# Performance work log

Measured on AMD Instinct MI355X. Metric: run time of the kernel, lower is better.

## Reference

```python
import jax, jax.numpy as jnp
import numpy as np

# N: batch rows of x, D: inner dim, E: output columns of sparse A, PER_COL: nnz per column
N, D, E, PER_COL = 64, 4096, 8192, 128
NNZ = E * PER_COL  # 1,048,576 nonzeros, stored sorted by column (CSC-like)


def setup_inputs() -> dict:
    key = jax.random.key(0)
    k1, k2, k3 = jax.random.split(key, 3)
    x = jax.random.normal(k1, (N, D), dtype=jnp.float32)
    values = jax.random.normal(k2, (NNZ,), dtype=jnp.float32)  # A.values (log-space entries)
    rows = jax.random.randint(k3, (NNZ,), 0, D, dtype=jnp.int32)  # A.indices[0]: row id in D
    # A.indices[1] / col_indptrs: column-sorted segment ids; every column non-empty
    col_ids = jnp.repeat(jnp.arange(E, dtype=jnp.int32), PER_COL)
    return {"x": x, "values": values, "rows": rows, "col_ids": col_ids}


def reference(x, values, rows, col_ids):
    # expansion[k, n] = A.values[k] + x[n, rows[k]]   (nnz leading so segment ops apply)
    expansion = values[:, None] + x.T[rows]                       # [NNZ, N]
    # segment max over each column's nnz block (== segment_csr(..., 'max'))
    m = jax.ops.segment_max(expansion, col_ids, num_segments=E)   # [E, N]
    # stable sum-exp offset by per-segment max, then log (== segment_csr(..., 'sum'))
    s = jax.ops.segment_sum(jnp.exp(expansion - m[col_ids]), col_ids, num_segments=E)  # [E, N]
    return (m + jnp.log(s)).T                                     # [N, E]
```

## Files before the change

### kernel.cpp

```cpp
#include <hip/hip_runtime.h>

#define NB  64
#define D_  4096
#define E_  8192
#define PC_ 128

#define LOG2E 1.4426950408889634f
#define LN2   0.6931471805599453f


typedef float vfloat2 __attribute__((ext_vector_type(2)));
#if __has_builtin(__builtin_amdgcn_cvt_pk_f32_fp8) && \
    __has_builtin(__builtin_amdgcn_cvt_pk_fp8_f32)
#define HW_FP8 1
#else
#define HW_FP8 0
#endif

__device__ __forceinline__ unsigned enc_e4m3(float y) {
    unsigned b = __float_as_uint(y);
    int t = (int)((b + 0x00080000u) >> 20) - 960;
    t = (t < 8) ? 0 : t;
    t = (t > 127) ? 127 : t;
    return (unsigned)t;
}
__device__ __forceinline__ float dec_e4m3(unsigned u) {
    return (u >= 8u) ? __uint_as_float((u + 960u) << 20) : 0.0f;
}

__global__ __launch_bounds__(256) void k_prep(const float* __restrict__ x,
                                              const float* __restrict__ values,
                                              const int*   __restrict__ rows,
                                              unsigned* __restrict__ y4,
                                              int2*     __restrict__ meta) {
    const int b = blockIdx.x;
    if (b < D_ / 64) {
        __shared__ float ld[64][65];
        const int wv = threadIdx.x >> 6, lane = threadIdx.x & 63;
        const int d0 = b * 64;
#pragma unroll
        for (int jj = 0; jj < 16; ++jj) {
            int n = wv + 4 * jj;
            ld[lane][n] = x[n * D_ + d0 + lane];
        }
        __syncthreads();
#pragma unroll
        for (int it = 0; it < 4; ++it) {
            int item = it * 256 + threadIdx.x;
            int dd = item >> 4, j = item & 15;
            float e0  = __builtin_amdgcn_exp2f(ld[dd][j]      * LOG2E);
            float e16 = __builtin_amdgcn_exp2f(ld[dd][j + 16] * LOG2E);
            float e32 = __builtin_amdgcn_exp2f(ld[dd][j + 32] * LOG2E);
            float e48 = __builtin_amdgcn_exp2f(ld[dd][j + 48] * LOG2E);
            unsigned p;
#if HW_FP8
            p = __builtin_amdgcn_cvt_pk_fp8_f32(e0,  e16, 0, false);
            p = __builtin_amdgcn_cvt_pk_fp8_f32(e32, e48, p, true);
#else
            p = enc_e4m3(e0) | (enc_e4m3(e16) << 8) |
                (enc_e4m3(e32) << 16) | (enc_e4m3(e48) << 24);
#endif
            y4[(d0 + dd) * 16 + j] = p;
        }
    } else {
        int i = (b - D_ / 64) * 1024 + threadIdx.x * 4;
        int4   r4 = *(const int4*)(rows + i);
        float4 v4 = *(const float4*)(values + i);
        int4 s0, s1;
        s0.x = r4.x; s0.y = __float_as_int(__builtin_amdgcn_exp2f(v4.x * LOG2E));
        s0.z = r4.y; s0.w = __float_as_int(__builtin_amdgcn_exp2f(v4.y * LOG2E));
        s1.x = r4.z; s1.y = __float_as_int(__builtin_amdgcn_exp2f(v4.z * LOG2E));
        s1.z = r4.w; s1.w = __float_as_int(__builtin_amdgcn_exp2f(v4.w * LOG2E));
        ((int4*)(meta + i))[0] = s0;
        ((int4*)(meta + i))[1] = s1;
    }
}

__global__ __launch_bounds__(256, 4) void k_acc(const unsigned* __restrict__ y4,
                                                const int2*  __restrict__ meta,
                                                float* __restrict__ out) {
    const int wv   = threadIdx.x >> 6;
    const int lane = threadIdx.x & 63;
    const int q    = lane >> 4;
    const int j    = lane & 15;
    const int e    = blockIdx.x * 4 + wv;
    const int2* __restrict__ mp = meta + e * PC_ + 32 * q;

    int4 mm[16];
#pragma unroll
    for (int u = 0; u < 16; ++u)
        mm[u] = *(const int4*)(mp + 2 * u);

    float ax = 0.f, ay = 0.f, az = 0.f, aw = 0.f;
#pragma unroll
    for (int u = 0; u < 16; ++u) {
        unsigned g0 = y4[((unsigned)mm[u].x << 4) + j];
        unsigned g1 = y4[((unsigned)mm[u].z << 4) + j];
        float w0 = __int_as_float(mm[u].y);
        float w1 = __int_as_float(mm[u].w);
#if HW_FP8
        vfloat2 a01 = __builtin_amdgcn_cvt_pk_f32_fp8(g0, false);
        vfloat2 a23 = __builtin_amdgcn_cvt_pk_f32_fp8(g0, true);
        vfloat2 b01 = __builtin_amdgcn_cvt_pk_f32_fp8(g1, false);
        vfloat2 b23 = __builtin_amdgcn_cvt_pk_f32_fp8(g1, true);
        float a0 = a01[0], a1 = a01[1], a2 = a23[0], a3 = a23[1];
        float b0 = b01[0], b1 = b01[1], b2 = b23[0], b3 = b23[1];
#else
        float a0 = dec_e4m3(g0 & 0xff), a1 = dec_e4m3((g0 >> 8) & 0xff);
        float a2 = dec_e4m3((g0 >> 16) & 0xff), a3 = dec_e4m3(g0 >> 24);
        float b0 = dec_e4m3(g1 & 0xff), b1 = dec_e4m3((g1 >> 8) & 0xff);
        float b2 = dec_e4m3((g1 >> 16) & 0xff), b3 = dec_e4m3(g1 >> 24);
#endif
        ax = __builtin_fmaf(w0, a0, ax);
        ay = __builtin_fmaf(w0, a1, ay);
        az = __builtin_fmaf(w0, a2, az);
        aw = __builtin_fmaf(w0, a3, aw);
        ax = __builtin_fmaf(w1, b0, ax);
        ay = __builtin_fmaf(w1, b1, ay);
        az = __builtin_fmaf(w1, b2, az);
        aw = __builtin_fmaf(w1, b3, aw);
    }

    ax += __shfl_xor(ax, 16); ax += __shfl_xor(ax, 32);
    ay += __shfl_xor(ay, 16); ay += __shfl_xor(ay, 32);
    az += __shfl_xor(az, 16); az += __shfl_xor(az, 32);
    aw += __shfl_xor(aw, 16); aw += __shfl_xor(aw, 32);

    if (q == 0) {
        out[j        * E_ + e] = LN2 * __builtin_amdgcn_logf(ax);
        out[(j + 16) * E_ + e] = LN2 * __builtin_amdgcn_logf(ay);
        out[(j + 32) * E_ + e] = LN2 * __builtin_amdgcn_logf(az);
        out[(j + 48) * E_ + e] = LN2 * __builtin_amdgcn_logf(aw);
    }
}

extern "C" void kernel_launch(void* const* d_in, const int* in_sizes, int n_in,
                              void* d_out, int out_size, void* d_ws, size_t ws_size,
                              hipStream_t stream) {
    const float* x      = (const float*)d_in[0];
    const float* values = (const float*)d_in[1];
    const int*   rows   = (const int*)d_in[2];
    float* out = (float*)d_out;

    char* ws = (char*)d_ws;
    unsigned* y4   = (unsigned*)ws;
    int2*     meta = (int2*)(ws + (512 << 10));

    k_prep<<<D_ / 64 + (E_ * PC_) / 1024, 256, 0, stream>>>(x, values, rows, y4, meta);
    k_acc <<<E_ / 4, 256, 0, stream>>>(y4, meta, out);
}
```

Baseline: 22.24 us.

## Bucket column nonzeros by row chunk and gather from LDS-staged tiles

The prep kernel now sorts each column's nonzeros into four row-range buckets using shared-memory atomic counters, with a fixed capacity per bucket and padding to multiples of eight. The accumulate kernel runs 1024-thread blocks covering 32 columns each. It stages one 64KB chunk of the packed fp8 exp(x) table into LDS at a time, and each wave walks its bucket of nonzeros against that chunk. The aim is to turn random global/L2 gathers into LDS gathers. The costs are a doubled metadata footprint, only one block per CU, extra barriers, and entries silently clamped if any bucket exceeds its capacity of 64.

```diff
diff --git a/kernel.cpp b/kernel.cpp
--- a/kernel.cpp
+++ b/kernel.cpp
@@ -8,6 +8,11 @@
 #define LOG2E 1.4426950408889634f
 #define LN2   0.6931471805599453f
 
+
+#define CH_LOG  10
+#define CH_ROWS 1024
+#define NCH     4
+#define CAP     64
 
 typedef float vfloat2 __attribute__((ext_vector_type(2)));
 #if __has_builtin(__builtin_amdgcn_cvt_pk_f32_fp8) && \
@@ -32,7 +37,8 @@
                                               const float* __restrict__ values,
                                               const int*   __restrict__ rows,
                                               unsigned* __restrict__ y4,
-                                              int2*     __restrict__ meta) {
+                                              unsigned* __restrict__ counts,
+                                              int2*     __restrict__ msort) {
     const int b = blockIdx.x;
     if (b < D_ / 64) {
         __shared__ float ld[64][65];
@@ -63,74 +69,137 @@
             y4[(d0 + dd) * 16 + j] = p;
         }
     } else {
-        int i = (b - D_ / 64) * 1024 + threadIdx.x * 4;
-        int4   r4 = *(const int4*)(rows + i);
-        float4 v4 = *(const float4*)(values + i);
-        int4 s0, s1;
-        s0.x = r4.x; s0.y = __float_as_int(__builtin_amdgcn_exp2f(v4.x * LOG2E));
-        s0.z = r4.y; s0.w = __float_as_int(__builtin_amdgcn_exp2f(v4.y * LOG2E));
-        s1.x = r4.z; s1.y = __float_as_int(__builtin_amdgcn_exp2f(v4.z * LOG2E));
-        s1.z = r4.w; s1.w = __float_as_int(__builtin_amdgcn_exp2f(v4.w * LOG2E));
-        ((int4*)(meta + i))[0] = s0;
-        ((int4*)(meta + i))[1] = s1;
+        __shared__ int cnts[4][NCH];
+        const int wv = threadIdx.x >> 6, lane = threadIdx.x & 63;
+        const int e = (b - D_ / 64) * 4 + wv;
+        if (lane < NCH) cnts[wv][lane] = 0;
+        __syncthreads();
+
+        const int base = e * PC_;
+        int   rA = rows[base + lane],      rB = rows[base + 64 + lane];
+        float wA = __builtin_amdgcn_exp2f(values[base + lane]      * LOG2E);
+        float wB = __builtin_amdgcn_exp2f(values[base + 64 + lane] * LOG2E);
+        int cA = rA >> CH_LOG, cB = rB >> CH_LOG;
+        int sA = atomicAdd(&cnts[wv][cA], 1);
+        int sB = atomicAdd(&cnts[wv][cB], 1);
+        sA = min(sA, CAP - 1); sB = min(sB, CAP - 1);
+        int2* mcol = msort + e * (NCH * CAP);
+        mcol[cA * CAP + sA] = make_int2(rA, __float_as_int(wA));
+        mcol[cB * CAP + sB] = make_int2(rB, __float_as_int(wB));
+        __syncthreads();
+
+        if (lane < 32) {
+            int c = lane >> 3, p = lane & 7;
+            int cnt = cnts[wv][c];
+            int padded = (cnt + 7) & ~7;
+            if (cnt + p < padded)
+                mcol[c * CAP + cnt + p] = make_int2(c << CH_LOG, 0);
+        }
+        if (lane == 0) {
+            unsigned t0 = (unsigned)(cnts[wv][0] + 7) >> 3;
+            unsigned t1 = (unsigned)(cnts[wv][1] + 7) >> 3;
+            unsigned t2 = (unsigned)(cnts[wv][2] + 7) >> 3;
+            unsigned t3 = (unsigned)(cnts[wv][3] + 7) >> 3;
+            counts[e] = t0 | (t1 << 8) | (t2 << 16) | (t3 << 24);
+        }
     }
 }
 
-__global__ __launch_bounds__(256, 4) void k_acc(const unsigned* __restrict__ y4,
-                                                const int2*  __restrict__ meta,
-                                                float* __restrict__ out) {
-    const int wv   = threadIdx.x >> 6;
-    const int lane = threadIdx.x & 63;
+__global__ __launch_bounds__(1024, 1) void k_acc(const unsigned* __restrict__ y4,
+                                                 const unsigned* __restrict__ counts,
+                                                 const int2*  __restrict__ msort,
+                                                 float* __restrict__ out) {
+    __shared__ unsigned ylds[CH_ROWS * 16];
+    const int tid  = threadIdx.x;
+    const int wv   = tid >> 6;
+    const int lane = tid & 63;
     const int q    = lane >> 4;
     const int j    = lane & 15;
-    const int e    = blockIdx.x * 4 + wv;
-    const int2* __restrict__ mp = meta + e * PC_ + 32 * q;
-
-    int4 mm[16];
+    const int e0   = blockIdx.x * 32 + wv;
+    const int e1   = e0 + 16;
+
+    const unsigned cp0 = counts[e0], cp1 = counts[e1];
+    const int2* __restrict__ m0 = msort + e0 * (NCH * CAP);
+    const int2* __restrict__ m1 = msort + e1 * (NCH * CAP);
+
+    float a0x = 0.f, a0y = 0.f, a0z = 0.f, a0w = 0.f;
+    float a1x = 0.f, a1y = 0.f, a1z = 0.f, a1w = 0.f;
+
+    for (int c = 0; c < NCH; ++c) {
+        __syncthreads();
+        {
+            const uint4* __restrict__ src =
+                (const uint4*)(y4 + c * (CH_ROWS * 16));
+            uint4* dst = (uint4*)ylds;
 #pragma unroll
-    for (int u = 0; u < 16; ++u)
-        mm[u] = *(const int4*)(mp + 2 * u);
-
-    float ax = 0.f, ay = 0.f, az = 0.f, aw = 0.f;
-#pragma unroll
-    for (int u = 0; u < 16; ++u) {
-        unsigned g0 = y4[((unsigned)mm[u].x << 4) + j];
-        unsigned g1 = y4[((unsigned)mm[u].z << 4) + j];
-        float w0 = __int_as_float(mm[u].y);
-        float w1 = __int_as_float(mm[u].w);
+            for (int r = 0; r < 4; ++r)
+                dst[tid + r * 1024] = src[tid + r * 1024];
+        }
+        __syncthreads();
+
+#define WALK(MP, CP, AX, AY, AZ, AW)                                          \
+        {                                                                     \
+            const int T = (int)((CP >> (8 * c)) & 0xffu);                     \
+            const int2* __restrict__ mc = MP + c * CAP;                       \
+            for (int t = 0; t < T; ++t) {                                     \
+                int4 m4 = *(const int4*)(mc + 8 * t + 2 * q);                 \
+                unsigned gA = ylds[(((unsigned)m4.x & (CH_ROWS - 1)) << 4) + j];\
+                unsigned gB = ylds[(((unsigned)m4.z & (CH_ROWS - 1)) << 4) + j];\
+                float w0 = __int_as_float(m4.y);                              \
+                float w1 = __int_as_float(m4.w);                              \
+                float A0, A1, A2, A3, B0, B1, B2, B3;                         \
+                {                                                             \
+                                                                  \
+                  _Pragma("clang diagnostic push")                            \
+                  A0 = A1 = A2 = A3 = B0 = B1 = B2 = B3 = 0.f;                \
+                  _Pragma("clang diagnostic pop")                             \
+                }                                                             \
+                DEC4(gA, A0, A1, A2, A3);                                     \
+                DEC4(gB, B0, B1, B2, B3);                                     \
+                AX = __builtin_fmaf(w0, A0, AX);                              \
+                AY = __builtin_fmaf(w0, A1, AY);                              \
+                AZ = __builtin_fmaf(w0, A2, AZ);                              \
+                AW = __builtin_fmaf(w0, A3, AW);                              \
+                AX = __builtin_fmaf(w1, B0, AX);                              \
+                AY = __builtin_fmaf(w1, B1, AY);                              \
+                AZ = __builtin_fmaf(w1, B2, AZ);                              \
+                AW = __builtin_fmaf(w1, B3, AW);                              \
+            }                                                                 \
+        }
 #if HW_FP8
-        vfloat2 a01 = __builtin_amdgcn_cvt_pk_f32_fp8(g0, false);
-        vfloat2 a23 = __builtin_amdgcn_cvt_pk_f32_fp8(g0, true);
-        vfloat2 b01 = __builtin_amdgcn_cvt_pk_f32_fp8(g1, false);
-        vfloat2 b23 = __builtin_amdgcn_cvt_pk_f32_fp8(g1, true);
-        float a0 = a01[0], a1 = a01[1], a2 = a23[0], a3 = a23[1];
-        float b0 = b01[0], b1 = b01[1], b2 = b23[0], b3 = b23[1];
+#define DEC4(G, D0, D1, D2, D3)                                               \
+        { vfloat2 lo = __builtin_amdgcn_cvt_pk_f32_fp8((G), false);           \
+          vfloat2 hi = __builtin_amdgcn_cvt_pk_f32_fp8((G), true);            \
+          D0 = lo[0]; D1 = lo[1]; D2 = hi[0]; D3 = hi[1]; }
 #else
-        float a0 = dec_e4m3(g0 & 0xff), a1 = dec_e4m3((g0 >> 8) & 0xff);
-        float a2 = dec_e4m3((g0 >> 16) & 0xff), a3 = dec_e4m3(g0 >> 24);
-        float b0 = dec_e4m3(g1 & 0xff), b1 = dec_e4m3((g1 >> 8) & 0xff);
-        float b2 = dec_e4m3((g1 >> 16) & 0xff), b3 = dec_e4m3(g1 >> 24);
+#define DEC4(G, D0, D1, D2, D3)                                               \
+        { D0 = dec_e4m3((G) & 0xff);        D1 = dec_e4m3(((G) >> 8) & 0xff); \
+          D2 = dec_e4m3(((G) >> 16) & 0xff); D3 = dec_e4m3((G) >> 24); }
 #endif
-        ax = __builtin_fmaf(w0, a0, ax);
-        ay = __builtin_fmaf(w0, a1, ay);
-        az = __builtin_fmaf(w0, a2, az);
-        aw = __builtin_fmaf(w0, a3, aw);
-        ax = __builtin_fmaf(w1, b0, ax);
-        ay = __builtin_fmaf(w1, b1, ay);
-        az = __builtin_fmaf(w1, b2, az);
-        aw = __builtin_fmaf(w1, b3, aw);
+        WALK(m0, cp0, a0x, a0y, a0z, a0w)
+        WALK(m1, cp1, a1x, a1y, a1z, a1w)
+#undef DEC4
+#undef WALK
     }
 
-    ax += __shfl_xor(ax, 16); ax += __shfl_xor(ax, 32);
-    ay += __shfl_xor(ay, 16); ay += __shfl_xor(ay, 32);
-    az += __shfl_xor(az, 16); az += __shfl_xor(az, 32);
-    aw += __shfl_xor(aw, 16); aw += __shfl_xor(aw, 32);
+    a0x += __shfl_xor(a0x, 16); a0x += __shfl_xor(a0x, 32);
+    a0y += __shfl_xor(a0y, 16); a0y += __shfl_xor(a0y, 32);
+    a0z += __shfl_xor(a0z, 16); a0z += __shfl_xor(a0z, 32);
+    a0w += __shfl_xor(a0w, 16); a0w += __shfl_xor(a0w, 32);
+    a1x += __shfl_xor(a1x, 16); a1x += __shfl_xor(a1x, 32);
+    a1y += __shfl_xor(a1y, 16); a1y += __shfl_xor(a1y, 32);
+    a1z += __shfl_xor(a1z, 16); a1z += __shfl_xor(a1z, 32);
+    a1w += __shfl_xor(a1w, 16); a1w += __shfl_xor(a1w, 32);
 
     if (q == 0) {
-        out[j        * E_ + e] = LN2 * __builtin_amdgcn_logf(ax);
-        out[(j + 16) * E_ + e] = LN2 * __builtin_amdgcn_logf(ay);
-        out[(j + 32) * E_ + e] = LN2 * __builtin_amdgcn_logf(az);
-        out[(j + 48) * E_ + e] = LN2 * __builtin_amdgcn_logf(aw);
+        out[j        * E_ + e0] = LN2 * __builtin_amdgcn_logf(a0x);
+        out[(j + 16) * E_ + e0] = LN2 * __builtin_amdgcn_logf(a0y);
+        out[(j + 32) * E_ + e0] = LN2 * __builtin_amdgcn_logf(a0z);
+        out[(j + 48) * E_ + e0] = LN2 * __builtin_amdgcn_logf(a0w);
+        out[j        * E_ + e1] = LN2 * __builtin_amdgcn_logf(a1x);
+        out[(j + 16) * E_ + e1] = LN2 * __builtin_amdgcn_logf(a1y);
+        out[(j + 32) * E_ + e1] = LN2 * __builtin_amdgcn_logf(a1z);
+        out[(j + 48) * E_ + e1] = LN2 * __builtin_amdgcn_logf(a1w);
     }
 }
 
@@ -143,9 +212,10 @@
     float* out = (float*)d_out;
 
     char* ws = (char*)d_ws;
-    unsigned* y4   = (unsigned*)ws;
-    int2*     meta = (int2*)(ws + (512 << 10));
-
-    k_prep<<<D_ / 64 + (E_ * PC_) / 1024, 256, 0, stream>>>(x, values, rows, y4, meta);
-    k_acc <<<E_ / 4, 256, 0, stream>>>(y4, meta, out);
-}
+    unsigned* y4     = (unsigned*)ws;
+    unsigned* counts = (unsigned*)(ws + (256 << 10));
+    int2*     msort  = (int2*)(ws + (512 << 10));
+
+    k_prep<<<D_ / 64 + E_ / 4, 256, 0, stream>>>(x, values, rows, y4, counts, msort);
+    k_acc <<<256, 1024, 0, stream>>>(y4, counts, msort, out);
+}
```

New measurement: 30.19 us. 1.36x slower.

## Stage half-batch fp8 exp table in LDS and gather from shared memory

Applied to the files above, without the earlier changes.

The fp8 exp(x) table is split into two batch halves, each 128KB, so that a whole half fits in LDS. A new 1024-thread kernel copies one half into shared memory and then runs its per-column gathers from LDS instead of global/L2. Each wave now handles two columns with eight lanes per row group, which changes the reduction and output indexing. The cost is re-staging 128KB per block across 512 blocks, plus reading the metadata twice (once per half), with only one block resident per CU.

```diff
diff --git a/kernel.cpp b/kernel.cpp
--- a/kernel.cpp
+++ b/kernel.cpp
@@ -28,10 +28,21 @@
     return (u >= 8u) ? __uint_as_float((u + 960u) << 20) : 0.0f;
 }
 
+#if HW_FP8
+#define DEC4(G, D0, D1, D2, D3)                                         \
+    { vfloat2 lo_ = __builtin_amdgcn_cvt_pk_f32_fp8((G), false);        \
+      vfloat2 hi_ = __builtin_amdgcn_cvt_pk_f32_fp8((G), true);         \
+      D0 = lo_[0]; D1 = lo_[1]; D2 = hi_[0]; D3 = hi_[1]; }
+#else
+#define DEC4(G, D0, D1, D2, D3)                                         \
+    { D0 = dec_e4m3((G) & 0xff);         D1 = dec_e4m3(((G) >> 8) & 0xff); \
+      D2 = dec_e4m3(((G) >> 16) & 0xff); D3 = dec_e4m3((G) >> 24); }
+#endif
+
 __global__ __launch_bounds__(256) void k_prep(const float* __restrict__ x,
                                               const float* __restrict__ values,
                                               const int*   __restrict__ rows,
-                                              unsigned* __restrict__ y4,
+                                              unsigned* __restrict__ yH,
                                               int2*     __restrict__ meta) {
     const int b = blockIdx.x;
     if (b < D_ / 64) {
@@ -47,20 +58,22 @@
 #pragma unroll
         for (int it = 0; it < 4; ++it) {
             int item = it * 256 + threadIdx.x;
-            int dd = item >> 4, j = item & 15;
-            float e0  = __builtin_amdgcn_exp2f(ld[dd][j]      * LOG2E);
-            float e16 = __builtin_amdgcn_exp2f(ld[dd][j + 16] * LOG2E);
-            float e32 = __builtin_amdgcn_exp2f(ld[dd][j + 32] * LOG2E);
-            float e48 = __builtin_amdgcn_exp2f(ld[dd][j + 48] * LOG2E);
+            int dd = item >> 4, rem = item & 15;
+            int h = rem >> 3, j = rem & 7;
+            int n0 = 32 * h + j;
+            float e0 = __builtin_amdgcn_exp2f(ld[dd][n0]      * LOG2E);
+            float e1 = __builtin_amdgcn_exp2f(ld[dd][n0 + 8]  * LOG2E);
+            float e2 = __builtin_amdgcn_exp2f(ld[dd][n0 + 16] * LOG2E);
+            float e3 = __builtin_amdgcn_exp2f(ld[dd][n0 + 24] * LOG2E);
             unsigned p;
 #if HW_FP8
-            p = __builtin_amdgcn_cvt_pk_fp8_f32(e0,  e16, 0, false);
-            p = __builtin_amdgcn_cvt_pk_fp8_f32(e32, e48, p, true);
+            p = __builtin_amdgcn_cvt_pk_fp8_f32(e0, e1, 0, false);
+            p = __builtin_amdgcn_cvt_pk_fp8_f32(e2, e3, p, true);
 #else
-            p = enc_e4m3(e0) | (enc_e4m3(e16) << 8) |
-                (enc_e4m3(e32) << 16) | (enc_e4m3(e48) << 24);
+            p = enc_e4m3(e0) | (enc_e4m3(e1) << 8) |
+                (enc_e4m3(e2) << 16) | (enc_e4m3(e3) << 24);
 #endif
-            y4[(d0 + dd) * 16 + j] = p;
+            yH[h * (D_ * 8) + (d0 + dd) * 8 + j] = p;
         }
     } else {
         int i = (b - D_ / 64) * 1024 + threadIdx.x * 4;
@@ -76,61 +89,73 @@
     }
 }
 
-__global__ __launch_bounds__(256, 4) void k_acc(const unsigned* __restrict__ y4,
-                                                const int2*  __restrict__ meta,
-                                                float* __restrict__ out) {
-    const int wv   = threadIdx.x >> 6;
-    const int lane = threadIdx.x & 63;
-    const int q    = lane >> 4;
-    const int j    = lane & 15;
-    const int e    = blockIdx.x * 4 + wv;
-    const int2* __restrict__ mp = meta + e * PC_ + 32 * q;
+__global__ __launch_bounds__(1024) void k_walk(const unsigned* __restrict__ yH,
+                                               const int2*  __restrict__ meta,
+                                               float* __restrict__ out) {
+    __shared__ uint4 lds4[D_ * 8 / 4];
+    const unsigned* ylds = (const unsigned*)lds4;
+    const int tid  = threadIdx.x;
+    const int half = blockIdx.x >> 8;
+    const int cb   = (blockIdx.x & 255) * 32;
 
-    int4 mm[16];
+    {
+        const uint4* __restrict__ src = (const uint4*)(yH + half * (D_ * 8));
 #pragma unroll
-    for (int u = 0; u < 16; ++u)
-        mm[u] = *(const int4*)(mp + 2 * u);
+        for (int r = 0; r < 8; ++r)
+            lds4[tid + r * 1024] = src[tid + r * 1024];
+    }
+    __syncthreads();
 
-    float ax = 0.f, ay = 0.f, az = 0.f, aw = 0.f;
+    const int wv   = tid >> 6;
+    const int lane = tid & 63;
+    const int q    = lane >> 3;
+    const int j    = lane & 7;
+    const int e0   = cb + wv * 2, e1 = e0 + 1;
+    const int2* __restrict__ mp0 = meta + e0 * PC_ + q;
+    const int2* __restrict__ mp1 = meta + e1 * PC_ + q;
+
+    float a00 = 0.f, a01 = 0.f, a02 = 0.f, a03 = 0.f;
+    float a10 = 0.f, a11 = 0.f, a12 = 0.f, a13 = 0.f;
 #pragma unroll
-    for (int u = 0; u < 16; ++u) {
-        unsigned g0 = y4[((unsigned)mm[u].x << 4) + j];
-        unsigned g1 = y4[((unsigned)mm[u].z << 4) + j];
-        float w0 = __int_as_float(mm[u].y);
-        float w1 = __int_as_float(mm[u].w);
-#if HW_FP8
-        vfloat2 a01 = __builtin_amdgcn_cvt_pk_f32_fp8(g0, false);
-        vfloat2 a23 = __builtin_amdgcn_cvt_pk_f32_fp8(g0, true);
-        vfloat2 b01 = __builtin_amdgcn_cvt_pk_f32_fp8(g1, false);
-        vfloat2 b23 = __builtin_amdgcn_cvt_pk_f32_fp8(g1, true);
-        float a0 = a01[0], a1 = a01[1], a2 = a23[0], a3 = a23[1];
-        float b0 = b01[0], b1 = b01[1], b2 = b23[0], b3 = b23[1];
-#else
-        float a0 = dec_e4m3(g0 & 0xff), a1 = dec_e4m3((g0 >> 8) & 0xff);
-        float a2 = dec_e4m3((g0 >> 16) & 0xff), a3 = dec_e4m3(g0 >> 24);
-        float b0 = dec_e4m3(g1 & 0xff), b1 = dec_e4m3((g1 >> 8) & 0xff);
-        float b2 = dec_e4m3((g1 >> 16) & 0xff), b3 = dec_e4m3(g1 >> 24);
-#endif
-        ax = __builtin_fmaf(w0, a0, ax);
-        ay = __builtin_fmaf(w0, a1, ay);
-        az = __builtin_fmaf(w0, a2, az);
-        aw = __builtin_fmaf(w0, a3, aw);
-        ax = __builtin_fmaf(w1, b0, ax);
-        ay = __builtin_fmaf(w1, b1, ay);
-        az = __builtin_fmaf(w1, b2, az);
-        aw = __builtin_fmaf(w1, b3, aw);
+    for (int t = 0; t < PC_ / 8; ++t) {
+        int2 m0 = mp0[8 * t];
+        int2 m1 = mp1[8 * t];
+        unsigned g0 = ylds[(((unsigned)m0.x) << 3) + j];
+        unsigned g1 = ylds[(((unsigned)m1.x) << 3) + j];
+        float w0 = __int_as_float(m0.y);
+        float w1 = __int_as_float(m1.y);
+        float f0, f1, f2, f3;
+        DEC4(g0, f0, f1, f2, f3);
+        a00 = __builtin_fmaf(w0, f0, a00);
+        a01 = __builtin_fmaf(w0, f1, a01);
+        a02 = __builtin_fmaf(w0, f2, a02);
+        a03 = __builtin_fmaf(w0, f3, a03);
+        DEC4(g1, f0, f1, f2, f3);
+        a10 = __builtin_fmaf(w1, f0, a10);
+        a11 = __builtin_fmaf(w1, f1, a11);
+        a12 = __builtin_fmaf(w1, f2, a12);
+        a13 = __builtin_fmaf(w1, f3, a13);
     }
 
-    ax += __shfl_xor(ax, 16); ax += __shfl_xor(ax, 32);
-    ay += __shfl_xor(ay, 16); ay += __shfl_xor(ay, 32);
-    az += __shfl_xor(az, 16); az += __shfl_xor(az, 32);
-    aw += __shfl_xor(aw, 16); aw += __shfl_xor(aw, 32);
+    a00 += __shfl_xor(a00, 8); a00 += __shfl_xor(a00, 16); a00 += __shfl_xor(a00, 32);
+    a01 += __shfl_xor(a01, 8); a01 += __shfl_xor(a01, 16); a01 += __shfl_xor(a01, 32);
+    a02 += __shfl_xor(a02, 8); a02 += __shfl_xor(a02, 16); a02 += __shfl_xor(a02, 32);
+    a03 += __shfl_xor(a03, 8); a03 += __shfl_xor(a03, 16); a03 += __shfl_xor(a03, 32);
+    a10 += __shfl_xor(a10, 8); a10 += __shfl_xor(a10, 16); a10 += __shfl_xor(a10, 32);
+    a11 += __shfl_xor(a11, 8); a11 += __shfl_xor(a11, 16); a11 += __shfl_xor(a11, 32);
+    a12 += __shfl_xor(a12, 8); a12 += __shfl_xor(a12, 16); a12 += __shfl_xor(a12, 32);
+    a13 += __shfl_xor(a13, 8); a13 += __shfl_xor(a13, 16); a13 += __shfl_xor(a13, 32);
 
     if (q == 0) {
-        out[j        * E_ + e] = LN2 * __builtin_amdgcn_logf(ax);
-        out[(j + 16) * E_ + e] = LN2 * __builtin_amdgcn_logf(ay);
-        out[(j + 32) * E_ + e] = LN2 * __builtin_amdgcn_logf(az);
-        out[(j + 48) * E_ + e] = LN2 * __builtin_amdgcn_logf(aw);
+        const int nb = 32 * half + j;
+        out[nb        * E_ + e0] = LN2 * __builtin_amdgcn_logf(a00);
+        out[(nb +  8) * E_ + e0] = LN2 * __builtin_amdgcn_logf(a01);
+        out[(nb + 16) * E_ + e0] = LN2 * __builtin_amdgcn_logf(a02);
+        out[(nb + 24) * E_ + e0] = LN2 * __builtin_amdgcn_logf(a03);
+        out[nb        * E_ + e1] = LN2 * __builtin_amdgcn_logf(a10);
+        out[(nb +  8) * E_ + e1] = LN2 * __builtin_amdgcn_logf(a11);
+        out[(nb + 16) * E_ + e1] = LN2 * __builtin_amdgcn_logf(a12);
+        out[(nb + 24) * E_ + e1] = LN2 * __builtin_amdgcn_logf(a13);
     }
 }
 
@@ -143,9 +168,9 @@
     float* out = (float*)d_out;
 
     char* ws = (char*)d_ws;
-    unsigned* y4   = (unsigned*)ws;
-    int2*     meta = (int2*)(ws + (512 << 10));
+    unsigned* yH   = (unsigned*)ws;
+    int2*     meta = (int2*)(ws + (256 << 10));
 
-    k_prep<<<D_ / 64 + (E_ * PC_) / 1024, 256, 0, stream>>>(x, values, rows, y4, meta);
-    k_acc <<<E_ / 4, 256, 0, stream>>>(y4, meta, out);
+    k_prep<<<D_ / 64 + (E_ * PC_) / 1024, 256, 0, stream>>>(x, values, rows, yH, meta);
+    k_walk<<<512, 1024, 0, stream>>>(yH, meta, out);
 }
```

Result: slower. 24.90 us (+12.0%).

## Fuse value exponentiation into accumulate kernel, drop meta workspace pass

Applied to the files above, without the earlier changes.

The prep kernel no longer builds an interleaved (row, exp(value)) meta array. The accumulate kernel now reads rows and values directly and computes exp(value) inline. This removes a write and re-read of 8 MB of intermediate data and shrinks the prep grid to just the x-packing blocks. In exchange, each column's exponentials are recomputed per lane-group, adding extra transcendental work in the hot kernel.

```diff
diff --git a/kernel.cpp b/kernel.cpp
--- a/kernel.cpp
+++ b/kernel.cpp
@@ -28,97 +28,99 @@
     return (u >= 8u) ? __uint_as_float((u + 960u) << 20) : 0.0f;
 }
 
-__global__ __launch_bounds__(256) void k_prep(const float* __restrict__ x,
-                                              const float* __restrict__ values,
-                                              const int*   __restrict__ rows,
-                                              unsigned* __restrict__ y4,
-                                              int2*     __restrict__ meta) {
-    const int b = blockIdx.x;
-    if (b < D_ / 64) {
-        __shared__ float ld[64][65];
-        const int wv = threadIdx.x >> 6, lane = threadIdx.x & 63;
-        const int d0 = b * 64;
+#if HW_FP8
+#define DEC4(G, D0, D1, D2, D3)                                         \
+    { vfloat2 lo_ = __builtin_amdgcn_cvt_pk_f32_fp8((G), false);        \
+      vfloat2 hi_ = __builtin_amdgcn_cvt_pk_f32_fp8((G), true);         \
+      D0 = lo_[0]; D1 = lo_[1]; D2 = hi_[0]; D3 = hi_[1]; }
+#else
+#define DEC4(G, D0, D1, D2, D3)                                         \
+    { D0 = dec_e4m3((G) & 0xff);         D1 = dec_e4m3(((G) >> 8) & 0xff); \
+      D2 = dec_e4m3(((G) >> 16) & 0xff); D3 = dec_e4m3((G) >> 24); }
+#endif
+
+__global__ __launch_bounds__(256) void k_pack(const float* __restrict__ x,
+                                              unsigned* __restrict__ y4) {
+    __shared__ float ld[64][65];
+    const int wv = threadIdx.x >> 6, lane = threadIdx.x & 63;
+    const int d0 = blockIdx.x * 64;
 #pragma unroll
-        for (int jj = 0; jj < 16; ++jj) {
-            int n = wv + 4 * jj;
-            ld[lane][n] = x[n * D_ + d0 + lane];
-        }
-        __syncthreads();
+    for (int jj = 0; jj < 16; ++jj) {
+        int n = wv + 4 * jj;
+        ld[lane][n] = x[n * D_ + d0 + lane];
+    }
+    __syncthreads();
 #pragma unroll
-        for (int it = 0; it < 4; ++it) {
-            int item = it * 256 + threadIdx.x;
-            int dd = item >> 4, j = item & 15;
-            float e0  = __builtin_amdgcn_exp2f(ld[dd][j]      * LOG2E);
-            float e16 = __builtin_amdgcn_exp2f(ld[dd][j + 16] * LOG2E);
-            float e32 = __builtin_amdgcn_exp2f(ld[dd][j + 32] * LOG2E);
-            float e48 = __builtin_amdgcn_exp2f(ld[dd][j + 48] * LOG2E);
-            unsigned p;
+    for (int it = 0; it < 4; ++it) {
+        int item = it * 256 + threadIdx.x;
+        int dd = item >> 4, j = item & 15;
+        float e0  = __builtin_amdgcn_exp2f(ld[dd][j]      * LOG2E);
+        float e16 = __builtin_amdgcn_exp2f(ld[dd][j + 16] * LOG2E);
+        float e32 = __builtin_amdgcn_exp2f(ld[dd][j + 32] * LOG2E);
+        float e48 = __builtin_amdgcn_exp2f(ld[dd][j + 48] * LOG2E);
+        unsigned p;
 #if HW_FP8
-            p = __builtin_amdgcn_cvt_pk_fp8_f32(e0,  e16, 0, false);
-            p = __builtin_amdgcn_cvt_pk_fp8_f32(e32, e48, p, true);
+        p = __builtin_amdgcn_cvt_pk_fp8_f32(e0,  e16, 0, false);
+        p = __builtin_amdgcn_cvt_pk_fp8_f32(e32, e48, p, true);
 #else
-            p = enc_e4m3(e0) | (enc_e4m3(e16) << 8) |
-                (enc_e4m3(e32) << 16) | (enc_e4m3(e48) << 24);
+        p = enc_e4m3(e0) | (enc_e4m3(e16) << 8) |
+            (enc_e4m3(e32) << 16) | (enc_e4m3(e48) << 24);
 #endif
-            y4[(d0 + dd) * 16 + j] = p;
-        }
-    } else {
-        int i = (b - D_ / 64) * 1024 + threadIdx.x * 4;
-        int4   r4 = *(const int4*)(rows + i);
-        float4 v4 = *(const float4*)(values + i);
-        int4 s0, s1;
-        s0.x = r4.x; s0.y = __float_as_int(__builtin_amdgcn_exp2f(v4.x * LOG2E));
-        s0.z = r4.y; s0.w = __float_as_int(__builtin_amdgcn_exp2f(v4.y * LOG2E));
-        s1.x = r4.z; s1.y = __float_as_int(__builtin_amdgcn_exp2f(v4.z * LOG2E));
-        s1.z = r4.w; s1.w = __float_as_int(__builtin_amdgcn_exp2f(v4.w * LOG2E));
-        ((int4*)(meta + i))[0] = s0;
-        ((int4*)(meta + i))[1] = s1;
+        y4[(d0 + dd) * 16 + j] = p;
     }
 }
 
 __global__ __launch_bounds__(256, 4) void k_acc(const unsigned* __restrict__ y4,
-                                                const int2*  __restrict__ meta,
+                                                const float* __restrict__ values,
+                                                const int*   __restrict__ rows,
                                                 float* __restrict__ out) {
     const int wv   = threadIdx.x >> 6;
     const int lane = threadIdx.x & 63;
     const int q    = lane >> 4;
     const int j    = lane & 15;
     const int e    = blockIdx.x * 4 + wv;
-    const int2* __restrict__ mp = meta + e * PC_ + 32 * q;
+    const int base = e * PC_ + 32 * q;
 
-    int4 mm[16];
+    const int4*   __restrict__ rp = (const int4*)(rows + base);
+    const float4* __restrict__ vp = (const float4*)(values + base);
+
+    int4   r4[8];
+    float4 v4[8];
 #pragma unroll
-    for (int u = 0; u < 16; ++u)
-        mm[u] = *(const int4*)(mp + 2 * u);
+    for (int u = 0; u < 8; ++u) { r4[u] = rp[u]; v4[u] = vp[u]; }
 
     float ax = 0.f, ay = 0.f, az = 0.f, aw = 0.f;
 #pragma unroll
-    for (int u = 0; u < 16; ++u) {
-        unsigned g0 = y4[((unsigned)mm[u].x << 4) + j];
-        unsigned g1 = y4[((unsigned)mm[u].z << 4) + j];
-        float w0 = __int_as_float(mm[u].y);
-        float w1 = __int_as_float(mm[u].w);
-#if HW_FP8
-        vfloat2 a01 = __builtin_amdgcn_cvt_pk_f32_fp8(g0, false);
-        vfloat2 a23 = __builtin_amdgcn_cvt_pk_f32_fp8(g0, true);
-        vfloat2 b01 = __builtin_amdgcn_cvt_pk_f32_fp8(g1, false);
-        vfloat2 b23 = __builtin_amdgcn_cvt_pk_f32_fp8(g1, true);
-        float a0 = a01[0], a1 = a01[1], a2 = a23[0], a3 = a23[1];
-        float b0 = b01[0], b1 = b01[1], b2 = b23[0], b3 = b23[1];
-#else
-        float a0 = dec_e4m3(g0 & 0xff), a1 = dec_e4m3((g0 >> 8) & 0xff);
-        float a2 = dec_e4m3((g0 >> 16) & 0xff), a3 = dec_e4m3(g0 >> 24);
-        float b0 = dec_e4m3(g1 & 0xff), b1 = dec_e4m3((g1 >> 8) & 0xff);
-        float b2 = dec_e4m3((g1 >> 16) & 0xff), b3 = dec_e4m3(g1 >> 24);
-#endif
-        ax = __builtin_fmaf(w0, a0, ax);
-        ay = __builtin_fmaf(w0, a1, ay);
-        az = __builtin_fmaf(w0, a2, az);
-        aw = __builtin_fmaf(w0, a3, aw);
-        ax = __builtin_fmaf(w1, b0, ax);
-        ay = __builtin_fmaf(w1, b1, ay);
-        az = __builtin_fmaf(w1, b2, az);
-        aw = __builtin_fmaf(w1, b3, aw);
+    for (int u = 0; u < 8; ++u) {
+        unsigned g0 = y4[((unsigned)r4[u].x << 4) + j];
+        unsigned g1 = y4[((unsigned)r4[u].y << 4) + j];
+        unsigned g2 = y4[((unsigned)r4[u].z << 4) + j];
+        unsigned g3 = y4[((unsigned)r4[u].w << 4) + j];
+        float w0 = __builtin_amdgcn_exp2f(v4[u].x * LOG2E);
+        float w1 = __builtin_amdgcn_exp2f(v4[u].y * LOG2E);
+        float w2 = __builtin_amdgcn_exp2f(v4[u].z * LOG2E);
+        float w3 = __builtin_amdgcn_exp2f(v4[u].w * LOG2E);
+        float f0, f1, f2, f3;
+        DEC4(g0, f0, f1, f2, f3);
+        ax = __builtin_fmaf(w0, f0, ax);
+        ay = __builtin_fmaf(w0, f1, ay);
+        az = __builtin_fmaf(w0, f2, az);
+        aw = __builtin_fmaf(w0, f3, aw);
+        DEC4(g1, f0, f1, f2, f3);
+        ax = __builtin_fmaf(w1, f0, ax);
+        ay = __builtin_fmaf(w1, f1, ay);
+        az = __builtin_fmaf(w1, f2, az);
+        aw = __builtin_fmaf(w1, f3, aw);
+        DEC4(g2, f0, f1, f2, f3);
+        ax = __builtin_fmaf(w2, f0, ax);
+        ay = __builtin_fmaf(w2, f1, ay);
+        az = __builtin_fmaf(w2, f2, az);
+        aw = __builtin_fmaf(w2, f3, aw);
+        DEC4(g3, f0, f1, f2, f3);
+        ax = __builtin_fmaf(w3, f0, ax);
+        ay = __builtin_fmaf(w3, f1, ay);
+        az = __builtin_fmaf(w3, f2, az);
+        aw = __builtin_fmaf(w3, f3, aw);
     }
 
     ax += __shfl_xor(ax, 16); ax += __shfl_xor(ax, 32);
@@ -142,10 +144,8 @@
     const int*   rows   = (const int*)d_in[2];
     float* out = (float*)d_out;
 
-    char* ws = (char*)d_ws;
-    unsigned* y4   = (unsigned*)ws;
-    int2*     meta = (int2*)(ws + (512 << 10));
+    unsigned* y4 = (unsigned*)d_ws;
 
-    k_prep<<<D_ / 64 + (E_ * PC_) / 1024, 256, 0, stream>>>(x, values, rows, y4, meta);
-    k_acc <<<E_ / 4, 256, 0, stream>>>(y4, meta, out);
+    k_pack<<<D_ / 64, 256, 0, stream>>>(x, y4);
+    k_acc <<<E_ / 4, 256, 0, stream>>>(y4, values, rows, out);
 }
```

New measurement: 19.76 us. -11.2%, faster.
